# Optimization experiments

Measured on AMD Instinct MI355X. Metric: run time of the kernel, lower is better.

## Reference

```python
import jax, jax.numpy as jnp
import numpy as np

NUM_ITERS = 5
EPS = 1e-5


def setup_inputs() -> dict:
    key = jax.random.key(0)
    ks = jax.random.split(key, 5)
    C_in, C_out, D, H, W = 64, 64, 64, 256, 256
    return {
        "x": jax.random.normal(ks[0], (C_in, H, W), dtype=jnp.float32),
        "conv_w": jax.random.normal(ks[1], (C_out, C_in, 3, 3), dtype=jnp.float32) * 0.05,
        "conv_b": jax.random.normal(ks[2], (C_out,), dtype=jnp.float32) * 0.05,
        "bin_proj": jax.random.normal(ks[3], (C_out, D, 1), dtype=jnp.float32),
        "weight_matrix": jax.random.normal(ks[4], (C_out, D, D), dtype=jnp.float32),
        "gn_weight": jnp.ones((C_out,), dtype=jnp.float32),
        "gn_bias": jnp.zeros((C_out,), dtype=jnp.float32),
    }


def reference(x, conv_w, conv_b, bin_proj, weight_matrix, gn_weight, gn_bias):
    # query conv: (C_in,H,W) -> (C_out,H,W), SAME padding
    q = jax.lax.conv_general_dilated(
        x[None], conv_w, window_strides=(1, 1), padding="SAME",
        dimension_numbers=("NCHW", "OIHW", "NCHW"))[0]
    q = q + conv_b[:, None, None]

    bp = bin_proj[:, :, 0]  # (C, D) == bin_proj_c[:, 0] per channel
    # binary query / initial state: (C, H, W, D)
    state = jnp.sign(q[:, :, :, None] * bp[:, None, None, :])
    # unrolled Hopfield dynamics: state = sign(W_c @ state) per channel/pixel
    for _ in range(NUM_ITERS):
        state = jnp.sign(jnp.einsum("cde,chwe->chwd", weight_matrix, state))
    # readout: sum_d bp[c,d] * state[c,h,w,d] -> (C,H,W)
    out = jnp.einsum("cd,chwd->chw", bp, state)

    # GroupNorm(groups=1) over (C,H,W) with per-channel affine, then residual input is out+q
    y = out + q
    mean = jnp.mean(y)
    var = jnp.mean(jnp.square(y - mean))
    yn = (y - mean) * jax.lax.rsqrt(var + EPS)
    yn = yn * gn_weight[:, None, None] + gn_bias[:, None, None]
    return jax.nn.gelu(yn)
```

## Files before the change

kernel.cpp:

```cpp
#include <hip/hip_runtime.h>
#include <math.h>

#define N_TOT 4194304
#define CONV_BLOCKS 1024
#define XS_DW 5120
#define RSTRIDE 148
#define PITCH 272
#define PROWS 258
#define PCI (PROWS * PITCH)
#define PAD_TOT (64 * PCI)
#define PAD_BYTES (PAD_TOT * 4)
#define WS_PAD_OFF 32768

__device__ __forceinline__ float sgnf(float x) {
    return x > 0.f ? 1.f : (x < 0.f ? -1.f : 0.f);
}

__device__ __forceinline__ float gelu_f(float v) {
    const float c0 = 0.7978845608028654f;
    float inner = c0 * fmaf(0.044715f * v, v * v, v);
    return 0.5f * v * (1.f + tanhf(inner));
}

__device__ __forceinline__ void gll4(const float* g, float* l) {
    __builtin_amdgcn_global_load_lds((const __attribute__((address_space(1))) void*)g,
                                     (__attribute__((address_space(3))) void*)l, 4, 0, 0);
}
__device__ __forceinline__ void gll16(const float* g, float* l) {
    __builtin_amdgcn_global_load_lds((const __attribute__((address_space(1))) void*)g,
                                     (__attribute__((address_space(3))) void*)l, 16, 0, 0);
}

__global__ __launch_bounds__(64) void alpha_kernel(const float* __restrict__ bp,
                                                   const float* __restrict__ Wm,
                                                   float* __restrict__ alpha) {
    const int c = blockIdx.x, d = threadIdx.x;
    __shared__ float v[64];
    float bpv = bp[c * 64 + d];
    v[d] = sgnf(bpv);
    __syncthreads();
    const float* row = Wm + c * 4096 + d * 64;
    for (int it = 0; it < 5; ++it) {
        float s = 0.f;
        #pragma unroll
        for (int e = 0; e < 64; ++e) s = fmaf(row[e], v[e], s);
        __syncthreads();
        v[d] = sgnf(s);
        __syncthreads();
    }
    float val = bpv * v[d];
    #pragma unroll
    for (int off = 32; off; off >>= 1) val += __shfl_down(val, off);
    if (d == 0) alpha[c] = val;
}

__global__ __launch_bounds__(256) void pad_kernel(const float* __restrict__ x,
                                                  float* __restrict__ pad) {
    const int idx = blockIdx.x * 256 + threadIdx.x;
    const int ci = idx / PCI;
    int rem = idx - ci * PCI;
    const int py = rem / PITCH;
    const int px = rem - py * PITCH;
    float v = 0.f;
    if (py >= 1 && py <= 256 && px >= 1 && px <= 256)
        v = x[(ci << 16) + ((py - 1) << 8) + (px - 1)];
    pad[idx] = v;
}

#define LOAD_T(T, XSC, CIOFF)                                                 \
    {                                                                         \
        _Pragma("unroll")                                                     \
        for (int rr = 0; rr < 4; ++rr) {                                      \
            const int off_ = lrow + rr * RSTRIDE + (CIOFF);                   \
            float2 a_ = *reinterpret_cast<const float2*>(&(XSC)[off_]);       \
            float2 b_ = *reinterpret_cast<const float2*>(&(XSC)[off_ + 2]);   \
            T[rr][0] = a_.x; T[rr][1] = a_.y; T[rr][2] = b_.x; T[rr][3] = b_.y;\
        }                                                                     \
    }

#define FMA_CI(T, WP)                                                         \
    {                                                                         \
        _Pragma("unroll")                                                     \
        for (int co = 0; co < 4; ++co) {                                      \
            const float* w_ = (WP) + co * 576;                                \
            _Pragma("unroll")                                                 \
            for (int ky = 0; ky < 3; ++ky)                                    \
                _Pragma("unroll")                                             \
                for (int kx = 0; kx < 3; ++kx) {                              \
                    float wv_ = w_[ky * 3 + kx];                              \
                    _Pragma("unroll")                                         \
                    for (int dy = 0; dy < 2; ++dy)                            \
                        _Pragma("unroll")                                     \
                        for (int j = 0; j < 2; ++j)                           \
                            acc[co][dy][j] = fmaf(wv_, T[dy + ky][kx + j],    \
                                                  acc[co][dy][j]);            \
                }                                                             \
        }                                                                     \
    }

__global__ __launch_bounds__(256, 2) void conv_kernel(const float* __restrict__ xp,
                                                      const float* __restrict__ cw,
                                                      const float* __restrict__ cb,
                                                      const float* __restrict__ alpha,
                                                      float* __restrict__ y,
                                                      double* __restrict__ partials) {
    const int tid = threadIdx.x;
    const int b = blockIdx.x;
    const int tile = b & 63;
    const int cog = b >> 6;
    const int bx = tile & 7, by = tile >> 3;
    const int tx = tid & 15, ty = tid >> 4;

    __shared__ float xs[2][XS_DW];
    double* red = (double*)&xs[1][5032];

    int goff[5];
    #pragma unroll
    for (int i = 0; i < 5; ++i) {
        int c4 = i * 256 + tid;
        int r = c4 / 37;
        int rem = c4 - r * 37;
        int ci = rem / 9;
        int cc = rem - ci * 9;
        bool junk = (rem >= 36) || (c4 >= 1258);
        int g = ci * PCI + ((by << 5) + r) * PITCH + (bx << 5) + cc * 4;
        goff[i] = junk ? 0 : g;
    }

    float acc[4][2][2];
    #pragma unroll
    for (int co = 0; co < 4; ++co) {
        float bias = cb[cog * 4 + co];
        acc[co][0][0] = bias; acc[co][0][1] = bias;
        acc[co][1][0] = bias; acc[co][1][1] = bias;
    }

    #pragma unroll
    for (int i = 0; i < 5; ++i)
        gll16(xp + goff[i], &xs[0][(i * 256 + tid) * 4]);
    __syncthreads();

    const int lrow = (2 * ty) * RSTRIDE + 2 * tx;
    const float* wbase = cw + cog * 4 * 576;

    float tA[4][4], tB[4][4];

    for (int s = 0; s < 16; ++s) {
        const int cur = s & 1;
        if (s < 15) {
            const float* xb = xp + (s + 1) * (4 * PCI);
            #pragma unroll
            for (int i = 0; i < 5; ++i)
                gll16(xb + goff[i], &xs[cur ^ 1][(i * 256 + tid) * 4]);
        }

        const float* xsc = xs[cur];
        const float* wp = wbase + (s * 4) * 9;

        LOAD_T(tA, xsc, 0)
        LOAD_T(tB, xsc, 36)
        FMA_CI(tA, wp)
        LOAD_T(tA, xsc, 72)
        FMA_CI(tB, wp + 9)
        LOAD_T(tB, xsc, 108)
        FMA_CI(tA, wp + 18)
        FMA_CI(tB, wp + 27)

        __syncthreads();
    }

    double s1 = 0.0, s2 = 0.0;
    const int gx0 = (bx << 5) + 2 * tx;
    const int gy0 = (by << 5) + 2 * ty;
    #pragma unroll
    for (int co = 0; co < 4; ++co) {
        float a = alpha[cog * 4 + co];
        const int cb_off = (cog * 4 + co) << 16;
        #pragma unroll
        for (int dy = 0; dy < 2; ++dy) {
            float q0 = acc[co][dy][0];
            float q1 = acc[co][dy][1];
            float y0v = q0 + (q0 > 0.f ? a : (q0 < 0.f ? -a : 0.f));
            float y1v = q1 + (q1 > 0.f ? a : (q1 < 0.f ? -a : 0.f));
            float2 pk; pk.x = y0v; pk.y = y1v;
            *reinterpret_cast<float2*>(&y[cb_off + ((gy0 + dy) << 8) + gx0]) = pk;
            s1 += (double)y0v + (double)y1v;
            s2 += (double)y0v * (double)y0v + (double)y1v * (double)y1v;
        }
    }
    #pragma unroll
    for (int off = 32; off; off >>= 1) {
        s1 += __shfl_down(s1, off);
        s2 += __shfl_down(s2, off);
    }
    const int wid = tid >> 6;
    if ((tid & 63) == 0) { red[wid * 2] = s1; red[wid * 2 + 1] = s2; }
    __syncthreads();
    if (tid == 0) {
        double a1 = red[0] + red[2] + red[4] + red[6];
        double a2 = red[1] + red[3] + red[5] + red[7];
        partials[b * 2]     = a1;
        partials[b * 2 + 1] = a2;
    }
}

__global__ __launch_bounds__(256, 2) void conv_fb(const float* __restrict__ x,
                                                  const float* __restrict__ cw,
                                                  const float* __restrict__ cb,
                                                  const float* __restrict__ alpha,
                                                  const float* __restrict__ zbuf,
                                                  float* __restrict__ y,
                                                  double* __restrict__ partials) {
    const int tid = threadIdx.x;
    const int b = blockIdx.x;
    const int tile = b & 63;
    const int cog = b >> 6;
    const int bx = tile & 7, by = tile >> 3;
    const int tx = tid & 15, ty = tid >> 4;

    __shared__ float xs[2][4864];
    __shared__ double red[4][2];

    int voff[19];
    unsigned vmask = 0u;
    #pragma unroll
    for (int i = 0; i < 19; ++i) {
        int idx = i * 256 + tid;
        int r = idx / 136;
        int rem = idx - r * 136;
        int ci = rem / 34;
        int c = rem - ci * 34;
        int gy = (by << 5) - 1 + r;
        int gx = (bx << 5) + c - 1;
        bool ok = (idx < 4624) && ((unsigned)gy < 256u) && ((unsigned)gx < 256u);
        voff[i] = (ci << 16) + (gy << 8) + gx;
        if (ok) vmask |= (1u << i);
    }

    float acc[4][2][2];
    #pragma unroll
    for (int co = 0; co < 4; ++co) {
        float bias = cb[cog * 4 + co];
        acc[co][0][0] = bias; acc[co][0][1] = bias;
        acc[co][1][0] = bias; acc[co][1][1] = bias;
    }

    #pragma unroll
    for (int i = 0; i < 19; ++i) {
        const float* src = (vmask & (1u << i)) ? (x + voff[i]) : zbuf;
        gll4(src, &xs[0][i * 256 + tid]);
    }
    __syncthreads();

    const int lrow2 = (2 * ty) * 136 + 2 * tx;
    const float* wbase = cw + cog * 4 * 576;

    for (int s = 0; s < 16; ++s) {
        const int cur = s & 1;
        if (s < 15) {
            const float* xb = x + ((s + 1) << 18);
            #pragma unroll
            for (int i = 0; i < 19; ++i) {
                const float* src = (vmask & (1u << i)) ? (xb + voff[i]) : zbuf;
                gll4(src, &xs[cur ^ 1][i * 256 + tid]);
            }
        }
        const float* xsc = xs[cur];
        #pragma unroll
        for (int ci = 0; ci < 4; ++ci) {
            float t[4][4];
            #pragma unroll
            for (int rr = 0; rr < 4; ++rr) {
                const int off = lrow2 + rr * 136 + ci * 34;
                float2 a = *reinterpret_cast<const float2*>(&xsc[off]);
                float2 bb = *reinterpret_cast<const float2*>(&xsc[off + 2]);
                t[rr][0] = a.x; t[rr][1] = a.y; t[rr][2] = bb.x; t[rr][3] = bb.y;
            }
            const float* wp = wbase + (s * 4 + ci) * 9;
            #pragma unroll
            for (int co = 0; co < 4; ++co) {
                const float* w = wp + co * 576;
                #pragma unroll
                for (int ky = 0; ky < 3; ++ky)
                    #pragma unroll
                    for (int kx = 0; kx < 3; ++kx) {
                        float wv = w[ky * 3 + kx];
                        #pragma unroll
                        for (int dy = 0; dy < 2; ++dy)
                            #pragma unroll
                            for (int j = 0; j < 2; ++j)
                                acc[co][dy][j] = fmaf(wv, t[dy + ky][kx + j], acc[co][dy][j]);
                    }
            }
        }
        __syncthreads();
    }

    double s1 = 0.0, s2 = 0.0;
    const int gx0 = (bx << 5) + 2 * tx;
    const int gy0 = (by << 5) + 2 * ty;
    #pragma unroll
    for (int co = 0; co < 4; ++co) {
        float a = alpha[cog * 4 + co];
        const int cb_off = (cog * 4 + co) << 16;
        #pragma unroll
        for (int dy = 0; dy < 2; ++dy) {
            float q0 = acc[co][dy][0];
            float q1 = acc[co][dy][1];
            float y0v = q0 + (q0 > 0.f ? a : (q0 < 0.f ? -a : 0.f));
            float y1v = q1 + (q1 > 0.f ? a : (q1 < 0.f ? -a : 0.f));
            float2 pk; pk.x = y0v; pk.y = y1v;
            *reinterpret_cast<float2*>(&y[cb_off + ((gy0 + dy) << 8) + gx0]) = pk;
            s1 += (double)y0v + (double)y1v;
            s2 += (double)y0v * (double)y0v + (double)y1v * (double)y1v;
        }
    }
    #pragma unroll
    for (int off = 32; off; off >>= 1) {
        s1 += __shfl_down(s1, off);
        s2 += __shfl_down(s2, off);
    }
    const int wid = tid >> 6;
    if ((tid & 63) == 0) { red[wid][0] = s1; red[wid][1] = s2; }
    __syncthreads();
    if (tid == 0) {
        partials[b * 2]     = red[0][0] + red[1][0] + red[2][0] + red[3][0];
        partials[b * 2 + 1] = red[0][1] + red[1][1] + red[2][1] + red[3][1];
    }
}

__global__ __launch_bounds__(256) void stats_kernel(const double* __restrict__ partials,
                                                    float* __restrict__ stats) {
    const int tid = threadIdx.x;
    double s1 = 0.0, s2 = 0.0;
    for (int i = tid; i < CONV_BLOCKS; i += 256) {
        s1 += partials[2 * i];
        s2 += partials[2 * i + 1];
    }
    #pragma unroll
    for (int off = 32; off; off >>= 1) {
        s1 += __shfl_down(s1, off);
        s2 += __shfl_down(s2, off);
    }
    __shared__ double red[4][2];
    const int wid = tid >> 6;
    if ((tid & 63) == 0) { red[wid][0] = s1; red[wid][1] = s2; }
    __syncthreads();
    if (tid == 0) {
        double a1 = red[0][0] + red[1][0] + red[2][0] + red[3][0];
        double a2 = red[0][1] + red[1][1] + red[2][1] + red[3][1];
        double mean = a1 / (double)N_TOT;
        double var = a2 / (double)N_TOT - mean * mean;
        stats[0] = (float)mean;
        stats[1] = (float)(1.0 / sqrt(var + 1e-5));
    }
}

__global__ __launch_bounds__(256) void finalize_kernel(float* __restrict__ y,
                                                       const float* __restrict__ stats,
                                                       const float* __restrict__ gnw,
                                                       const float* __restrict__ gnb) {
    const int i = blockIdx.x * 256 + threadIdx.x;
    const float mean = stats[0], istd = stats[1];
    const int c = i >> 14;
    const float scale = gnw[c] * istd;
    const float shift = gnb[c] - mean * scale;
    float4 v = reinterpret_cast<float4*>(y)[i];
    v.x = gelu_f(fmaf(v.x, scale, shift));
    v.y = gelu_f(fmaf(v.y, scale, shift));
    v.z = gelu_f(fmaf(v.z, scale, shift));
    v.w = gelu_f(fmaf(v.w, scale, shift));
    reinterpret_cast<float4*>(y)[i] = v;
}

extern "C" void kernel_launch(void* const* d_in, const int* in_sizes, int n_in,
                              void* d_out, int out_size, void* d_ws, size_t ws_size,
                              hipStream_t stream) {
    const float* x   = (const float*)d_in[0];
    const float* cw  = (const float*)d_in[1];
    const float* cb  = (const float*)d_in[2];
    const float* bp  = (const float*)d_in[3];
    const float* Wm  = (const float*)d_in[4];
    const float* gnw = (const float*)d_in[5];
    const float* gnb = (const float*)d_in[6];
    float* out = (float*)d_out;

    char* ws = (char*)d_ws;
    float* alpha     = (float*)ws;
    float* stats     = (float*)(ws + 256);
    double* partials = (double*)(ws + 512);

    alpha_kernel<<<64, 64, 0, stream>>>(bp, Wm, alpha);

    if (ws_size >= (size_t)WS_PAD_OFF + PAD_BYTES) {
        float* xpad = (float*)(ws + WS_PAD_OFF);
        pad_kernel<<<PAD_TOT / 256, 256, 0, stream>>>(x, xpad);
        conv_kernel<<<CONV_BLOCKS, 256, 0, stream>>>(xpad, cw, cb, alpha, out, partials);
    } else {
        float* zbuf = (float*)(ws + 32768);
        hipMemsetAsync(zbuf, 0, 256, stream);
        conv_fb<<<CONV_BLOCKS, 256, 0, stream>>>(x, cw, cb, alpha, zbuf, out, partials);
    }

    stats_kernel<<<1, 256, 0, stream>>>(partials, stats);
    finalize_kernel<<<4096, 256, 0, stream>>>(out, stats, gnw, gnb);
}
```

Measured before the change: 91.87 us.

## Fuse conv, global stats and GELU finalize via cooperative grid sync

Adds a cooperative-launch conv kernel that keeps conv results in registers, writes per-block partial sums, grid-syncs, reduces the global mean and variance in every block, and then applies the normalization and GELU before a single store. This removes the separate stats and finalize launches and the extra read and write of the full output tensor. It requires all 1024 blocks to be co-resident. If the cooperative launch fails, it falls back to the old three-kernel path. The grid-wide barrier and the redundant per-block reduction of partials add some cost.

```diff
diff --git a/kernel.cpp b/kernel.cpp
--- a/kernel.cpp
+++ b/kernel.cpp
@@ -1,5 +1,8 @@
 #include <hip/hip_runtime.h>
+#include <hip/hip_cooperative_groups.h>
 #include <math.h>
+
+namespace cg = cooperative_groups;
 
 #define N_TOT 4194304
 #define CONV_BLOCKS 1024
@@ -98,76 +101,149 @@
         }                                                                     \
     }
 
+#define CONV_BODY(XP, CW, CB)                                                 \
+    const int tid = threadIdx.x;                                              \
+    const int b = blockIdx.x;                                                 \
+    const int tile = b & 63;                                                  \
+    const int cog = b >> 6;                                                   \
+    const int bx = tile & 7, by = tile >> 3;                                  \
+    const int tx = tid & 15, ty = tid >> 4;                                   \
+    __shared__ float xs[2][XS_DW];                                            \
+    double* red = (double*)&xs[1][5032];                                      \
+    int goff[5];                                                              \
+    _Pragma("unroll")                                                         \
+    for (int i = 0; i < 5; ++i) {                                             \
+        int c4 = i * 256 + tid;                                               \
+        int r = c4 / 37;                                                      \
+        int rem = c4 - r * 37;                                                \
+        int ci = rem / 9;                                                     \
+        int cc = rem - ci * 9;                                                \
+        bool junk = (rem >= 36) || (c4 >= 1258);                              \
+        int g = ci * PCI + ((by << 5) + r) * PITCH + (bx << 5) + cc * 4;      \
+        goff[i] = junk ? 0 : g;                                               \
+    }                                                                         \
+    float acc[4][2][2];                                                       \
+    _Pragma("unroll")                                                         \
+    for (int co = 0; co < 4; ++co) {                                          \
+        float bias = (CB)[cog * 4 + co];                                      \
+        acc[co][0][0] = bias; acc[co][0][1] = bias;                           \
+        acc[co][1][0] = bias; acc[co][1][1] = bias;                           \
+    }                                                                         \
+    _Pragma("unroll")                                                         \
+    for (int i = 0; i < 5; ++i)                                               \
+        gll16((XP) + goff[i], &xs[0][(i * 256 + tid) * 4]);                   \
+    __syncthreads();                                                          \
+    const int lrow = (2 * ty) * RSTRIDE + 2 * tx;                             \
+    const float* wbase = (CW) + cog * 4 * 576;                                \
+    float tA[4][4], tB[4][4];                                                 \
+    for (int s = 0; s < 16; ++s) {                                            \
+        const int cur = s & 1;                                                \
+        if (s < 15) {                                                         \
+            const float* xb = (XP) + (s + 1) * (4 * PCI);                     \
+            _Pragma("unroll")                                                 \
+            for (int i = 0; i < 5; ++i)                                       \
+                gll16(xb + goff[i], &xs[cur ^ 1][(i * 256 + tid) * 4]);       \
+        }                                                                     \
+        const float* xsc = xs[cur];                                           \
+        const float* wp = wbase + (s * 4) * 9;                                \
+        LOAD_T(tA, xsc, 0)                                                    \
+        LOAD_T(tB, xsc, 36)                                                   \
+        FMA_CI(tA, wp)                                                        \
+        LOAD_T(tA, xsc, 72)                                                   \
+        FMA_CI(tB, wp + 9)                                                    \
+        LOAD_T(tB, xsc, 108)                                                  \
+        FMA_CI(tA, wp + 18)                                                   \
+        FMA_CI(tB, wp + 27)                                                   \
+        __syncthreads();                                                      \
+    }
+
+__global__ __launch_bounds__(256, 2) void conv_coop(const float* __restrict__ xp,
+                                                    const float* __restrict__ cw,
+                                                    const float* __restrict__ cb,
+                                                    const float* __restrict__ alpha,
+                                                    const float* __restrict__ gnw,
+                                                    const float* __restrict__ gnb,
+                                                    float* __restrict__ y,
+                                                    double* __restrict__ partials) {
+    CONV_BODY(xp, cw, cb)
+
+    double s1 = 0.0, s2 = 0.0;
+    float av[4];
+    #pragma unroll
+    for (int co = 0; co < 4; ++co) {
+        av[co] = alpha[cog * 4 + co];
+        #pragma unroll
+        for (int dy = 0; dy < 2; ++dy)
+            #pragma unroll
+            for (int j = 0; j < 2; ++j) {
+                float q = acc[co][dy][j];
+                float yv = q + (q > 0.f ? av[co] : (q < 0.f ? -av[co] : 0.f));
+                s1 += (double)yv;
+                s2 += (double)yv * (double)yv;
+            }
+    }
+    #pragma unroll
+    for (int off = 32; off; off >>= 1) {
+        s1 += __shfl_down(s1, off);
+        s2 += __shfl_down(s2, off);
+    }
+    const int wid = tid >> 6;
+    if ((tid & 63) == 0) { red[wid * 2] = s1; red[wid * 2 + 1] = s2; }
+    __syncthreads();
+    if (tid == 0) {
+        partials[b * 2]     = red[0] + red[2] + red[4] + red[6];
+        partials[b * 2 + 1] = red[1] + red[3] + red[5] + red[7];
+    }
+    __threadfence();
+    cg::this_grid().sync();
+
+    double t1 = 0.0, t2 = 0.0;
+    for (int i = tid; i < CONV_BLOCKS; i += 256) {
+        t1 += partials[2 * i];
+        t2 += partials[2 * i + 1];
+    }
+    #pragma unroll
+    for (int off = 32; off; off >>= 1) {
+        t1 += __shfl_down(t1, off);
+        t2 += __shfl_down(t2, off);
+    }
+    if ((tid & 63) == 0) { red[wid * 2] = t1; red[wid * 2 + 1] = t2; }
+    __syncthreads();
+    double a1 = red[0] + red[2] + red[4] + red[6];
+    double a2 = red[1] + red[3] + red[5] + red[7];
+    double mean_d = a1 / (double)N_TOT;
+    double var = a2 / (double)N_TOT - mean_d * mean_d;
+    const float mean = (float)mean_d;
+    const float istd = (float)(1.0 / sqrt(var + 1e-5));
+
+    const int gx0 = (bx << 5) + 2 * tx;
+    const int gy0 = (by << 5) + 2 * ty;
+    #pragma unroll
+    for (int co = 0; co < 4; ++co) {
+        const float scale = gnw[cog * 4 + co] * istd;
+        const float shift = gnb[cog * 4 + co] - mean * scale;
+        const int cb_off = (cog * 4 + co) << 16;
+        #pragma unroll
+        for (int dy = 0; dy < 2; ++dy) {
+            float q0 = acc[co][dy][0];
+            float q1 = acc[co][dy][1];
+            float y0v = q0 + (q0 > 0.f ? av[co] : (q0 < 0.f ? -av[co] : 0.f));
+            float y1v = q1 + (q1 > 0.f ? av[co] : (q1 < 0.f ? -av[co] : 0.f));
+            float2 pk;
+            pk.x = gelu_f(fmaf(y0v, scale, shift));
+            pk.y = gelu_f(fmaf(y1v, scale, shift));
+            *reinterpret_cast<float2*>(&y[cb_off + ((gy0 + dy) << 8) + gx0]) = pk;
+        }
+    }
+}
+
 __global__ __launch_bounds__(256, 2) void conv_kernel(const float* __restrict__ xp,
                                                       const float* __restrict__ cw,
                                                       const float* __restrict__ cb,
                                                       const float* __restrict__ alpha,
                                                       float* __restrict__ y,
                                                       double* __restrict__ partials) {
-    const int tid = threadIdx.x;
-    const int b = blockIdx.x;
-    const int tile = b & 63;
-    const int cog = b >> 6;
-    const int bx = tile & 7, by = tile >> 3;
-    const int tx = tid & 15, ty = tid >> 4;
-
-    __shared__ float xs[2][XS_DW];
-    double* red = (double*)&xs[1][5032];
-
-    int goff[5];
-    #pragma unroll
-    for (int i = 0; i < 5; ++i) {
-        int c4 = i * 256 + tid;
-        int r = c4 / 37;
-        int rem = c4 - r * 37;
-        int ci = rem / 9;
-        int cc = rem - ci * 9;
-        bool junk = (rem >= 36) || (c4 >= 1258);
-        int g = ci * PCI + ((by << 5) + r) * PITCH + (bx << 5) + cc * 4;
-        goff[i] = junk ? 0 : g;
-    }
-
-    float acc[4][2][2];
-    #pragma unroll
-    for (int co = 0; co < 4; ++co) {
-        float bias = cb[cog * 4 + co];
-        acc[co][0][0] = bias; acc[co][0][1] = bias;
-        acc[co][1][0] = bias; acc[co][1][1] = bias;
-    }
-
-    #pragma unroll
-    for (int i = 0; i < 5; ++i)
-        gll16(xp + goff[i], &xs[0][(i * 256 + tid) * 4]);
-    __syncthreads();
-
-    const int lrow = (2 * ty) * RSTRIDE + 2 * tx;
-    const float* wbase = cw + cog * 4 * 576;
-
-    float tA[4][4], tB[4][4];
-
-    for (int s = 0; s < 16; ++s) {
-        const int cur = s & 1;
-        if (s < 15) {
-            const float* xb = xp + (s + 1) * (4 * PCI);
-            #pragma unroll
-            for (int i = 0; i < 5; ++i)
-                gll16(xb + goff[i], &xs[cur ^ 1][(i * 256 + tid) * 4]);
-        }
-
-        const float* xsc = xs[cur];
-        const float* wp = wbase + (s * 4) * 9;
-
-        LOAD_T(tA, xsc, 0)
-        LOAD_T(tB, xsc, 36)
-        FMA_CI(tA, wp)
-        LOAD_T(tA, xsc, 72)
-        FMA_CI(tB, wp + 9)
-        LOAD_T(tB, xsc, 108)
-        FMA_CI(tA, wp + 18)
-        FMA_CI(tB, wp + 27)
-
-        __syncthreads();
-    }
+    CONV_BODY(xp, cw, cb)
 
     double s1 = 0.0, s2 = 0.0;
     const int gx0 = (bx << 5) + 2 * tx;
@@ -197,11 +273,53 @@
     if ((tid & 63) == 0) { red[wid * 2] = s1; red[wid * 2 + 1] = s2; }
     __syncthreads();
     if (tid == 0) {
-        double a1 = red[0] + red[2] + red[4] + red[6];
-        double a2 = red[1] + red[3] + red[5] + red[7];
-        partials[b * 2]     = a1;
-        partials[b * 2 + 1] = a2;
-    }
+        partials[b * 2]     = red[0] + red[2] + red[4] + red[6];
+        partials[b * 2 + 1] = red[1] + red[3] + red[5] + red[7];
+    }
+}
+
+__global__ __launch_bounds__(256) void stats_kernel(const double* __restrict__ partials,
+                                                    float* __restrict__ stats) {
+    const int tid = threadIdx.x;
+    double s1 = 0.0, s2 = 0.0;
+    for (int i = tid; i < CONV_BLOCKS; i += 256) {
+        s1 += partials[2 * i];
+        s2 += partials[2 * i + 1];
+    }
+    #pragma unroll
+    for (int off = 32; off; off >>= 1) {
+        s1 += __shfl_down(s1, off);
+        s2 += __shfl_down(s2, off);
+    }
+    __shared__ double red[4][2];
+    const int wid = tid >> 6;
+    if ((tid & 63) == 0) { red[wid][0] = s1; red[wid][1] = s2; }
+    __syncthreads();
+    if (tid == 0) {
+        double a1 = red[0][0] + red[1][0] + red[2][0] + red[3][0];
+        double a2 = red[0][1] + red[1][1] + red[2][1] + red[3][1];
+        double mean = a1 / (double)N_TOT;
+        double var = a2 / (double)N_TOT - mean * mean;
+        stats[0] = (float)mean;
+        stats[1] = (float)(1.0 / sqrt(var + 1e-5));
+    }
+}
+
+__global__ __launch_bounds__(256) void finalize_kernel(float* __restrict__ y,
+                                                       const float* __restrict__ stats,
+                                                       const float* __restrict__ gnw,
+                                                       const float* __restrict__ gnb) {
+    const int i = blockIdx.x * 256 + threadIdx.x;
+    const float mean = stats[0], istd = stats[1];
+    const int c = i >> 14;
+    const float scale = gnw[c] * istd;
+    const float shift = gnb[c] - mean * scale;
+    float4 v = reinterpret_cast<float4*>(y)[i];
+    v.x = gelu_f(fmaf(v.x, scale, shift));
+    v.y = gelu_f(fmaf(v.y, scale, shift));
+    v.z = gelu_f(fmaf(v.z, scale, shift));
+    v.w = gelu_f(fmaf(v.w, scale, shift));
+    reinterpret_cast<float4*>(y)[i] = v;
 }
 
 __global__ __launch_bounds__(256, 2) void conv_fb(const float* __restrict__ x,
@@ -329,50 +447,6 @@
     }
 }
 
-__global__ __launch_bounds__(256) void stats_kernel(const double* __restrict__ partials,
-                                                    float* __restrict__ stats) {
-    const int tid = threadIdx.x;
-    double s1 = 0.0, s2 = 0.0;
-    for (int i = tid; i < CONV_BLOCKS; i += 256) {
-        s1 += partials[2 * i];
-        s2 += partials[2 * i + 1];
-    }
-    #pragma unroll
-    for (int off = 32; off; off >>= 1) {
-        s1 += __shfl_down(s1, off);
-        s2 += __shfl_down(s2, off);
-    }
-    __shared__ double red[4][2];
-    const int wid = tid >> 6;
-    if ((tid & 63) == 0) { red[wid][0] = s1; red[wid][1] = s2; }
-    __syncthreads();
-    if (tid == 0) {
-        double a1 = red[0][0] + red[1][0] + red[2][0] + red[3][0];
-        double a2 = red[0][1] + red[1][1] + red[2][1] + red[3][1];
-        double mean = a1 / (double)N_TOT;
-        double var = a2 / (double)N_TOT - mean * mean;
-        stats[0] = (float)mean;
-        stats[1] = (float)(1.0 / sqrt(var + 1e-5));
-    }
-}
-
-__global__ __launch_bounds__(256) void finalize_kernel(float* __restrict__ y,
-                                                       const float* __restrict__ stats,
-                                                       const float* __restrict__ gnw,
-                                                       const float* __restrict__ gnb) {
-    const int i = blockIdx.x * 256 + threadIdx.x;
-    const float mean = stats[0], istd = stats[1];
-    const int c = i >> 14;
-    const float scale = gnw[c] * istd;
-    const float shift = gnb[c] - mean * scale;
-    float4 v = reinterpret_cast<float4*>(y)[i];
-    v.x = gelu_f(fmaf(v.x, scale, shift));
-    v.y = gelu_f(fmaf(v.y, scale, shift));
-    v.z = gelu_f(fmaf(v.z, scale, shift));
-    v.w = gelu_f(fmaf(v.w, scale, shift));
-    reinterpret_cast<float4*>(y)[i] = v;
-}
-
 extern "C" void kernel_launch(void* const* d_in, const int* in_sizes, int n_in,
                               void* d_out, int out_size, void* d_ws, size_t ws_size,
                               hipStream_t stream) {
@@ -395,13 +469,22 @@
     if (ws_size >= (size_t)WS_PAD_OFF + PAD_BYTES) {
         float* xpad = (float*)(ws + WS_PAD_OFF);
         pad_kernel<<<PAD_TOT / 256, 256, 0, stream>>>(x, xpad);
-        conv_kernel<<<CONV_BLOCKS, 256, 0, stream>>>(xpad, cw, cb, alpha, out, partials);
+
+        void* args[] = {(void*)&xpad, (void*)&cw, (void*)&cb, (void*)&alpha,
+                        (void*)&gnw, (void*)&gnb, (void*)&out, (void*)&partials};
+        hipError_t e = hipLaunchCooperativeKernel((void*)conv_coop,
+                                                  dim3(CONV_BLOCKS), dim3(256),
+                                                  args, 0, stream);
+        if (e != hipSuccess) {
+            conv_kernel<<<CONV_BLOCKS, 256, 0, stream>>>(xpad, cw, cb, alpha, out, partials);
+            stats_kernel<<<1, 256, 0, stream>>>(partials, stats);
+            finalize_kernel<<<4096, 256, 0, stream>>>(out, stats, gnw, gnb);
+        }
     } else {
         float* zbuf = (float*)(ws + 32768);
         hipMemsetAsync(zbuf, 0, 256, stream);
         conv_fb<<<CONV_BLOCKS, 256, 0, stream>>>(x, cw, cb, alpha, zbuf, out, partials);
-    }
-
-    stats_kernel<<<1, 256, 0, stream>>>(partials, stats);
-    finalize_kernel<<<4096, 256, 0, stream>>>(out, stats, gnw, gnb);
-}
+        stats_kernel<<<1, 256, 0, stream>>>(partials, stats);
+        finalize_kernel<<<4096, 256, 0, stream>>>(out, stats, gnw, gnb);
+    }
+}
```

Result: slower. 292.4 us (+218.2%).
